# Kernel tuning notes

Hardware: AMD Instinct MI355X
Metric: run time of the kernel (lower is better)

The kernel has to match this reference:

```python
import jax, jax.numpy as jnp
import numpy as np

B, L, D_MODEL = 1, 1024, 768
H = 12            # num_heads == num_key_value_heads
FDIM = 16         # feature_dim
HEAD_DIM = D_MODEL // H  # 64
EPS = 1e-12
R2 = np.sqrt(2.0)
RD = np.sqrt(float(FDIM))        # sqrt(16) = 4
RRD = np.sqrt(RD)                # sqrt(4) = 2


def setup_inputs() -> dict:
    key = jax.random.key(0)
    ks = jax.random.split(key, 5)
    s = 1.0 / np.sqrt(D_MODEL)
    return {
        "hidden_states": jax.random.normal(ks[0], (B, L, D_MODEL), dtype=jnp.float32),
        "Wq": jax.random.normal(ks[1], (D_MODEL, H * FDIM), dtype=jnp.float32) * s,
        "Wk": jax.random.normal(ks[2], (D_MODEL, H * FDIM), dtype=jnp.float32) * s,
        "Wv": jax.random.normal(ks[3], (D_MODEL, D_MODEL), dtype=jnp.float32) * s,
        "Wo": jax.random.normal(ks[4], (D_MODEL, D_MODEL), dtype=jnp.float32) * s,
    }


def taylor_exp_feature_map(x):
    # x: (b, h, l, FDIM) -> (b, h, l, 1 + FDIM + FDIM^2)
    x2 = (x[..., :, None] * x[..., None, :]).reshape(*x.shape[:-1], FDIM * FDIM) / R2
    ones = jnp.ones((*x.shape[:-1], 1), dtype=x.dtype)
    return jnp.concatenate([ones, x / RRD, x2 / RD], axis=-1)


def reference(hidden_states, Wq, Wk, Wv, Wo):
    b, l, _ = hidden_states.shape
    q = (hidden_states @ Wq).reshape(b, l, H, FDIM).transpose(0, 2, 1, 3)
    k = (hidden_states @ Wk).reshape(b, l, H, FDIM).transpose(0, 2, 1, 3)
    v = (hidden_states @ Wv).reshape(b, l, H, HEAD_DIM).transpose(0, 2, 1, 3)
    q = taylor_exp_feature_map(q)  # (b,h,l,Dexp)
    k = taylor_exp_feature_map(k)  # (b,h,l,Dexp)
    # causal linear attention: y_t = q_t . cumsum_t(k_s v_s^T) / (q_t . cumsum_t(k_s) + eps)
    kv = k[..., :, None] * v[..., None, :]          # (b,h,l,Dexp,hd)
    kv_cum = jnp.cumsum(kv, axis=2)                  # (b,h,l,Dexp,hd)
    num = jnp.einsum('bhln,bhlnd->bhld', q, kv_cum)  # (b,h,l,hd)
    k_cum = jnp.cumsum(k, axis=2)                    # (b,h,l,Dexp)
    den = jnp.einsum('bhln,bhln->bhl', q, k_cum)[..., None] + EPS
    y = num / den                                    # (b,h,l,hd)
    y = y.transpose(0, 2, 1, 3).reshape(b, l, H * HEAD_DIM)
    return y @ Wo
```

## Files before the change

kernel.cpp:

```cpp
#include <hip/hip_runtime.h>

#define C2 0.17677669529663687f

typedef __attribute__((ext_vector_type(8))) short short8;
typedef __attribute__((ext_vector_type(8))) unsigned short ushort8;
typedef __attribute__((ext_vector_type(4))) float f32x4;

__device__ __forceinline__ unsigned short f2bf(float x) {
    union { float f; unsigned u; } v; v.f = x;
    unsigned r = v.u + 0x7fffu + ((v.u >> 16) & 1u);
    return (unsigned short)(r >> 16);
}
__device__ __forceinline__ float bf2f(unsigned short u) {
    union { unsigned u; float f; } v; v.u = ((unsigned)u) << 16;
    return v.f;
}

__device__ __forceinline__ void gemm_inblk_splitk(
    const float* __restrict__ A, const float* __restrict__ W,
    float* __restrict__ out, int row0, int n0, int outcol0, int ldw, int outld)
{
    __shared__ unsigned short Al[2][2][64][40];
    __shared__ unsigned short Bl[2][2][64][40];
    __shared__ float red[64][65];
    const int tid = threadIdx.x;
    const int g = tid >> 8;
    const int t = tid & 255;
    const int lane = t & 63, wave4 = t >> 6;
    const int wm = wave4 & 1, wn = wave4 >> 1;
    const int quad = lane >> 4, lr = lane & 15;
    const int k0base = g * 384;

    f32x4 acc[2][2] = {{{0.f,0.f,0.f,0.f},{0.f,0.f,0.f,0.f}},
                       {{0.f,0.f,0.f,0.f},{0.f,0.f,0.f,0.f}}};

    float4 ra[2], rb[2];
    #pragma unroll
    for (int l = 0; l < 2; ++l) {
        int idx = t + l * 256;
        ra[l] = *(const float4*)&A[(size_t)(row0 + (idx >> 3)) * 768 + k0base + (idx & 7) * 4];
        rb[l] = *(const float4*)&W[(size_t)(k0base + (idx >> 4)) * ldw + n0 + (idx & 15) * 4];
    }
    #pragma unroll
    for (int l = 0; l < 2; ++l) {
        int idx = t + l * 256;
        *(ushort4*)&Al[g][0][idx >> 3][(idx & 7) * 4] =
            make_ushort4(f2bf(ra[l].x), f2bf(ra[l].y), f2bf(ra[l].z), f2bf(ra[l].w));
        int kr = idx >> 4, nq = (idx & 15) * 4;
        int col = (((kr >> 3) ^ ((idx & 15) >> 2)) << 3) | (kr & 7);
        Bl[g][0][nq + 0][col] = f2bf(rb[l].x);
        Bl[g][0][nq + 1][col] = f2bf(rb[l].y);
        Bl[g][0][nq + 2][col] = f2bf(rb[l].z);
        Bl[g][0][nq + 3][col] = f2bf(rb[l].w);
    }
    __syncthreads();

    const int ITER = 12;
    #pragma unroll
    for (int i = 0; i < ITER; ++i) {
        const int cur = i & 1, nxt = cur ^ 1;
        float4 na[2], nb[2];
        if (i + 1 < ITER) {
            int kn = k0base + (i + 1) * 32;
            #pragma unroll
            for (int l = 0; l < 2; ++l) {
                int idx = t + l * 256;
                na[l] = *(const float4*)&A[(size_t)(row0 + (idx >> 3)) * 768 + kn + (idx & 7) * 4];
                nb[l] = *(const float4*)&W[(size_t)(kn + (idx >> 4)) * ldw + n0 + (idx & 15) * 4];
            }
        }
        short8 af[2], bfr[2];
        #pragma unroll
        for (int mi = 0; mi < 2; ++mi)
            af[mi] = *(const short8*)&Al[g][cur][wm * 32 + mi * 16 + lr][quad << 3];
        #pragma unroll
        for (int ni = 0; ni < 2; ++ni) {
            int csw = quad ^ ((wn * 2 + ni) & 3);
            bfr[ni] = *(const short8*)&Bl[g][cur][wn * 32 + ni * 16 + lr][csw << 3];
        }
        #pragma unroll
        for (int mi = 0; mi < 2; ++mi)
            #pragma unroll
            for (int ni = 0; ni < 2; ++ni)
                acc[mi][ni] = __builtin_amdgcn_mfma_f32_16x16x32_bf16(af[mi], bfr[ni], acc[mi][ni], 0, 0, 0);
        if (i + 1 < ITER) {
            #pragma unroll
            for (int l = 0; l < 2; ++l) {
                int idx = t + l * 256;
                *(ushort4*)&Al[g][nxt][idx >> 3][(idx & 7) * 4] =
                    make_ushort4(f2bf(na[l].x), f2bf(na[l].y), f2bf(na[l].z), f2bf(na[l].w));
                int kr = idx >> 4, nq = (idx & 15) * 4;
                int col = (((kr >> 3) ^ ((idx & 15) >> 2)) << 3) | (kr & 7);
                Bl[g][nxt][nq + 0][col] = f2bf(nb[l].x);
                Bl[g][nxt][nq + 1][col] = f2bf(nb[l].y);
                Bl[g][nxt][nq + 2][col] = f2bf(nb[l].z);
                Bl[g][nxt][nq + 3][col] = f2bf(nb[l].w);
            }
        }
        __syncthreads();
    }
    if (g == 1) {
        #pragma unroll
        for (int mi = 0; mi < 2; ++mi)
            #pragma unroll
            for (int ni = 0; ni < 2; ++ni)
                #pragma unroll
                for (int r = 0; r < 4; ++r)
                    red[wm * 32 + mi * 16 + quad * 4 + r][wn * 32 + ni * 16 + lr] = acc[mi][ni][r];
    }
    __syncthreads();
    if (g == 0) {
        #pragma unroll
        for (int mi = 0; mi < 2; ++mi)
            #pragma unroll
            for (int ni = 0; ni < 2; ++ni)
                #pragma unroll
                for (int r = 0; r < 4; ++r) {
                    int rr = wm * 32 + mi * 16 + quad * 4 + r;
                    int cc = wn * 32 + ni * 16 + lr;
                    out[(size_t)(row0 + rr) * outld + outcol0 + cc] = acc[mi][ni][r] + red[rr][cc];
                }
    }
}

__global__ __launch_bounds__(512) void gemm_qkv_mfma(
    const float* __restrict__ H, const float* __restrict__ Wq,
    const float* __restrict__ Wk, const float* __restrict__ Wv,
    float* __restrict__ out)
{
    const int nt = blockIdx.x, mt = blockIdx.y;
    const float* W; int ldw, n0;
    if (nt < 3)      { W = Wq; ldw = 192; n0 = nt * 64; }
    else if (nt < 6) { W = Wk; ldw = 192; n0 = (nt - 3) * 64; }
    else             { W = Wv; ldw = 768; n0 = (nt - 6) * 64; }
    gemm_inblk_splitk(H, W, out, mt * 64, n0, nt * 64, ldw, 1152);
}

__global__ __launch_bounds__(512) void gemm_wo_mfma(
    const float* __restrict__ Y, const float* __restrict__ Wo, float* __restrict__ out)
{
    const int nt = blockIdx.x, mt = blockIdx.y;
    gemm_inblk_splitk(Y, Wo, out, mt * 64, nt * 64, nt * 64, 768, 768);
}

__global__ __launch_bounds__(256) void chunk_state_k(
    const float* __restrict__ qkv, unsigned short* __restrict__ St, float* __restrict__ z)
{
    const int c = blockIdx.x, h = blockIdx.y;
    __shared__ float Kc[64][17];
    __shared__ unsigned short Pk[320][72];
    __shared__ unsigned short Vt[80][72];
    const int tid = threadIdx.x;
    const int lane = tid & 63, wave = tid >> 6;
    const int quad = lane >> 4, lr = lane & 15;

    {
        int s = tid >> 2, f4 = (tid & 3) * 4;
        float4 kv = *(const float4*)&qkv[(size_t)(c * 64 + s) * 1152 + 192 + h * 16 + f4];
        Kc[s][f4 + 0] = kv.x; Kc[s][f4 + 1] = kv.y; Kc[s][f4 + 2] = kv.z; Kc[s][f4 + 3] = kv.w;
    }
    #pragma unroll
    for (int l = 0; l < 4; ++l) {
        int idx = tid + l * 256;
        int s = idx >> 4, d4 = (idx & 15) * 4;
        float4 vv = *(const float4*)&qkv[(size_t)(c * 64 + s) * 1152 + 384 + h * 64 + d4];
        Vt[d4 + 0][s] = f2bf(vv.x);
        Vt[d4 + 1][s] = f2bf(vv.y);
        Vt[d4 + 2][s] = f2bf(vv.z);
        Vt[d4 + 3][s] = f2bf(vv.w);
    }
    for (int idx = tid; idx < 16 * 72; idx += 256) {
        int rr = 64 + idx / 72, ss = idx % 72;
        Vt[rr][ss] = (rr == 64 && ss < 64) ? (unsigned short)0x3F80 : (unsigned short)0;
    }
    __syncthreads();
    for (int idx = tid; idx < 2880; idx += 256) {
        int n = idx / 9, s8 = (idx % 9) * 8;
        short8 v8;
        #pragma unroll
        for (int tt = 0; tt < 8; ++tt) {
            int s = s8 + tt;
            float ph = 0.f;
            if (s < 64 && n < 273) {
                if (n == 0) ph = 1.f;
                else if (n < 17) ph = Kc[s][n - 1] * 0.5f;
                else { int m = n - 17; ph = Kc[s][m >> 4] * Kc[s][m & 15] * C2; }
            }
            v8[tt] = (short)f2bf(ph);
        }
        *(short8*)&Pk[n][s8] = v8;
    }
    __syncthreads();

    f32x4 acc[5][5];
    #pragma unroll
    for (int a = 0; a < 5; ++a)
        #pragma unroll
        for (int b = 0; b < 5; ++b) acc[a][b] = (f32x4){0.f, 0.f, 0.f, 0.f};
    #pragma unroll
    for (int ks = 0; ks < 2; ++ks) {
        short8 af[5], bfr[5];
        #pragma unroll
        for (int mt = 0; mt < 5; ++mt)
            af[mt] = *(const short8*)&Vt[mt * 16 + lr][ks * 32 + quad * 8];
        #pragma unroll
        for (int nt = 0; nt < 5; ++nt)
            bfr[nt] = *(const short8*)&Pk[(wave * 5 + nt) * 16 + lr][ks * 32 + quad * 8];
        #pragma unroll
        for (int mt = 0; mt < 5; ++mt)
            #pragma unroll
            for (int nt = 0; nt < 5; ++nt)
                acc[mt][nt] = __builtin_amdgcn_mfma_f32_16x16x32_bf16(af[mt], bfr[nt], acc[mt][nt], 0, 0, 0);
    }
    unsigned short* Sbt = St + (size_t)(h * 16 + c) * 18432;
    float* zb = z + (h * 16 + c) * 273;
    #pragma unroll
    for (int nt = 0; nt < 5; ++nt) {
        int n = (wave * 5 + nt) * 16 + lr;
        if (n < 273) {
            #pragma unroll
            for (int mt = 0; mt < 4; ++mt)
                #pragma unroll
                for (int r = 0; r < 4; ++r)
                    Sbt[(mt * 16 + quad * 4 + r) * 288 + n] = f2bf(acc[mt][nt][r]);
            if (quad == 0) zb[n] = acc[4][nt][0];
        }
    }
}

__global__ __launch_bounds__(256) void scan_state_k(unsigned short* __restrict__ St, float* __restrict__ z)
{
    const int NS = 12 * 64 * 273;
    int e = blockIdx.x * 256 + threadIdx.x;
    if (e < NS) {
        int hh = e / (64 * 273), rem = e % (64 * 273);
        int d = rem / 273, n = rem % 273;
        unsigned short* p = St + (size_t)hh * 16 * 18432 + d * 288 + n;
        float run = 0.f;
        #pragma unroll
        for (int c = 0; c < 16; ++c) {
            float v = bf2f(p[c * 18432]);
            p[c * 18432] = f2bf(run);
            run += v;
        }
    } else if (e < NS + 12 * 273) {
        int e2 = e - NS, hh = e2 / 273, n = e2 % 273;
        float* p = z + hh * 16 * 273 + n;
        float run = 0.f;
        #pragma unroll
        for (int c = 0; c < 16; ++c) { float v = p[c * 273]; p[c * 273] = run; run += v; }
    }
}

__global__ __launch_bounds__(256) void chunk_out_k(
    const float* __restrict__ qkv, const unsigned short* __restrict__ St, const float* __restrict__ z,
    float* __restrict__ y)
{
    const int c = blockIdx.x, h = blockIdx.y;
    __shared__ float Qc[64][17];
    __shared__ unsigned short Aq[64][40];
    __shared__ unsigned short Kb[64][40];
    __shared__ unsigned short Pq[64][360];
    __shared__ unsigned short Sv[64][360];
    __shared__ float zl[288];
    __shared__ float dpart[6][64];
    const int tid = threadIdx.x;
    const int lane = tid & 63, wave = tid >> 6;
    const int wm = wave & 1, wn = wave >> 1;
    const int quad = lane >> 4, lr = lane & 15;

    {
        int s = tid >> 2, f4 = (tid & 3) * 4;
        const float* base = &qkv[(size_t)(c * 64 + s) * 1152 + h * 16];
        float4 qv = *(const float4*)&base[f4];
        float4 kv = *(const float4*)&base[192 + f4];
        Qc[s][f4 + 0] = qv.x; Qc[s][f4 + 1] = qv.y; Qc[s][f4 + 2] = qv.z; Qc[s][f4 + 3] = qv.w;
        *(ushort4*)&Aq[s][f4] = make_ushort4(f2bf(qv.x), f2bf(qv.y), f2bf(qv.z), f2bf(qv.w));
        *(ushort4*)&Kb[s][f4] = make_ushort4(f2bf(kv.x), f2bf(kv.y), f2bf(kv.z), f2bf(kv.w));
        *(ushort4*)&Aq[s][16 + (tid & 3) * 4] = make_ushort4(0, 0, 0, 0);
        *(ushort4*)&Kb[s][16 + (tid & 3) * 4] = make_ushort4(0, 0, 0, 0);
    }
    #pragma unroll
    for (int l = 0; l < 4; ++l) {
        int idx = tid + l * 256;
        int s = idx >> 4, d4 = (idx & 15) * 4;
        float4 vv = *(const float4*)&qkv[(size_t)(c * 64 + s) * 1152 + 384 + h * 64 + d4];
        Sv[d4 + 0][288 + s] = f2bf(vv.x);
        Sv[d4 + 1][288 + s] = f2bf(vv.y);
        Sv[d4 + 2][288 + s] = f2bf(vv.z);
        Sv[d4 + 3][288 + s] = f2bf(vv.w);
    }
    const unsigned short* Sgt = St + (size_t)(h * 16 + c) * 18432;
    for (int idx = tid; idx < 64 * 34; idx += 256) {
        int d = idx / 34, n8 = (idx % 34) * 8;
        *(ushort8*)&Sv[d][n8] = *(const ushort8*)&Sgt[d * 288 + n8];
    }
    for (int idx = tid; idx < 64; idx += 256) Sv[idx][272] = Sgt[idx * 288 + 272];
    for (int idx = tid; idx < 64 * 15; idx += 256) {
        int d = idx / 15, n = 273 + idx % 15;
        Sv[d][n] = 0;
    }
    const float* zg = z + (h * 16 + c) * 273;
    for (int idx = tid; idx < 288; idx += 256) zl[idx] = (idx < 273) ? zg[idx] : 0.f;
    __syncthreads();

    f32x4 accS[2][2] = {{{0.f,0.f,0.f,0.f},{0.f,0.f,0.f,0.f}},
                        {{0.f,0.f,0.f,0.f},{0.f,0.f,0.f,0.f}}};
    {
        short8 af[2], bfr[2];
        #pragma unroll
        for (int mi = 0; mi < 2; ++mi)
            af[mi] = *(const short8*)&Aq[wm * 32 + mi * 16 + lr][quad * 8];
        #pragma unroll
        for (int ni = 0; ni < 2; ++ni)
            bfr[ni] = *(const short8*)&Kb[wn * 32 + ni * 16 + lr][quad * 8];
        #pragma unroll
        for (int mi = 0; mi < 2; ++mi)
            #pragma unroll
            for (int ni = 0; ni < 2; ++ni)
                accS[mi][ni] = __builtin_amdgcn_mfma_f32_16x16x32_bf16(af[mi], bfr[ni], accS[mi][ni], 0, 0, 0);
    }

    {
        int i = lane;
        float qr[16];
        #pragma unroll
        for (int f = 0; f < 16; ++f) qr[f] = Qc[i][f];
        float dp = 0.f;
        int n0 = wave * 72;
        for (int n = n0; n < n0 + 72; ++n) {
            float ph;
            if (n == 0) ph = 1.f;
            else if (n < 17) ph = qr[n - 1] * 0.5f;
            else if (n < 273) { int m = n - 17; ph = qr[m >> 4] * qr[m & 15] * C2; }
            else ph = 0.f;
            Pq[i][n] = f2bf(ph);
            dp += ph * zl[n];
        }
        dpart[wave][i] = dp;
    }

    #pragma unroll
    for (int mi = 0; mi < 2; ++mi) {
        float rs[4] = {0.f, 0.f, 0.f, 0.f};
        #pragma unroll
        for (int ni = 0; ni < 2; ++ni)
            #pragma unroll
            for (int r = 0; r < 4; ++r) {
                int i = wm * 32 + mi * 16 + quad * 4 + r;
                int j = wn * 32 + ni * 16 + lr;
                float u = accS[mi][ni][r];
                float sc = (j <= i) ? (1.f + 0.25f * u + u * u * (1.f / 32.f)) : 0.f;
                rs[r] += sc;
                Pq[i][288 + j] = f2bf(sc);
            }
        #pragma unroll
        for (int r = 0; r < 4; ++r) {
            float v = rs[r];
            v += __shfl_xor(v, 1);
            v += __shfl_xor(v, 2);
            v += __shfl_xor(v, 4);
            v += __shfl_xor(v, 8);
            if (lr == 0) dpart[4 + wn][wm * 32 + mi * 16 + quad * 4 + r] = v;
        }
    }
    __syncthreads();

    f32x4 acc[2][2] = {{{0.f,0.f,0.f,0.f},{0.f,0.f,0.f,0.f}},
                       {{0.f,0.f,0.f,0.f},{0.f,0.f,0.f,0.f}}};
    #pragma unroll
    for (int ks = 0; ks < 11; ++ks) {
        short8 af[2], bfr[2];
        #pragma unroll
        for (int mi = 0; mi < 2; ++mi)
            af[mi] = *(const short8*)&Pq[wm * 32 + mi * 16 + lr][ks * 32 + quad * 8];
        #pragma unroll
        for (int ni = 0; ni < 2; ++ni)
            bfr[ni] = *(const short8*)&Sv[wn * 32 + ni * 16 + lr][ks * 32 + quad * 8];
        #pragma unroll
        for (int mi = 0; mi < 2; ++mi)
            #pragma unroll
            for (int ni = 0; ni < 2; ++ni)
                acc[mi][ni] = __builtin_amdgcn_mfma_f32_16x16x32_bf16(af[mi], bfr[ni], acc[mi][ni], 0, 0, 0);
    }

    #pragma unroll
    for (int mi = 0; mi < 2; ++mi)
        #pragma unroll
        for (int r = 0; r < 4; ++r) {
            int i = wm * 32 + mi * 16 + quad * 4 + r;
            float den = dpart[0][i] + dpart[1][i] + dpart[2][i] +
                        dpart[3][i] + dpart[4][i] + dpart[5][i] + 1e-12f;
            float rden = 1.f / den;
            #pragma unroll
            for (int ni = 0; ni < 2; ++ni)
                y[(size_t)(c * 64 + i) * 768 + h * 64 + wn * 32 + ni * 16 + lr] = acc[mi][ni][r] * rden;
        }
}

extern "C" void kernel_launch(void* const* d_in, const int* in_sizes, int n_in,
                              void* d_out, int out_size, void* d_ws, size_t ws_size,
                              hipStream_t stream) {
    const float* hs = (const float*)d_in[0];
    const float* Wq = (const float*)d_in[1];
    const float* Wk = (const float*)d_in[2];
    const float* Wv = (const float*)d_in[3];
    const float* Wo = (const float*)d_in[4];
    float* out = (float*)d_out;
    float* ws  = (float*)d_ws;

    float* qkv = ws;
    float* yb  = ws + 1179648;
    unsigned short* St = (unsigned short*)(ws + 1966080);
    float* zb  = ws + 5320704;

    gemm_qkv_mfma<<<dim3(18, 16), 512, 0, stream>>>(hs, Wq, Wk, Wv, qkv);
    chunk_state_k<<<dim3(16, 12), 256, 0, stream>>>(qkv, St, zb);
    scan_state_k <<<832, 256, 0, stream>>>(St, zb);
    chunk_out_k  <<<dim3(16, 12), 256, 0, stream>>>(qkv, St, zb, yb);
    gemm_wo_mfma <<<dim3(12, 16), 512, 0, stream>>>(yb, Wo, out);
}
```

Measured before the change: 137.2 us.

## Fuse all five stages into one cooperative persistent kernel with grid syncs

Replaces the five separate launches (QKV GEMM, chunk state, scan, chunk output, Wo GEMM) with one cooperative kernel of 256 blocks that steps through the stages with grid.sync, sharing one union of LDS buffers. The goal is to remove per-launch overhead and the gaps between kernels. To fit the shared-memory union, chunk_out now runs its Pq/Sv feature GEMM in two smaller passes, and chunk_state is spread over 8 waves. The risks are that grid barriers cost time of their own, that the QKV GEMM now needs a second partial round (288 tasks on 256 blocks), and that larger LDS use per block can lower occupancy.

```diff
diff --git a/kernel.cpp b/kernel.cpp
--- a/kernel.cpp
+++ b/kernel.cpp
@@ -1,4 +1,7 @@
 #include <hip/hip_runtime.h>
+#include <hip/hip_cooperative_groups.h>
+
+namespace cg = cooperative_groups;
 
 #define C2 0.17677669529663687f
 
@@ -16,13 +19,16 @@
     return v.f;
 }
 
-__device__ __forceinline__ void gemm_inblk_splitk(
-    const float* __restrict__ A, const float* __restrict__ W,
+struct S1 { unsigned short Al[2][2][64][40]; unsigned short Bl[2][2][64][40]; float red[64][65]; };
+struct S2 { float Kc[64][17]; unsigned short Pk[320][72]; unsigned short Vt[80][72]; };
+struct S4 { float Qc[64][17]; float Kc[64][17]; unsigned short Pq[64][200]; unsigned short Sv[64][200];
+            float zl[288]; float dpart[6][64]; };
+union SMem { S1 s1; S2 s2; S4 s4; };
+
+__device__ __forceinline__ void gemm_body(
+    SMem& sm, const float* __restrict__ A, const float* __restrict__ W,
     float* __restrict__ out, int row0, int n0, int outcol0, int ldw, int outld)
 {
-    __shared__ unsigned short Al[2][2][64][40];
-    __shared__ unsigned short Bl[2][2][64][40];
-    __shared__ float red[64][65];
     const int tid = threadIdx.x;
     const int g = tid >> 8;
     const int t = tid & 255;
@@ -44,14 +50,14 @@
     #pragma unroll
     for (int l = 0; l < 2; ++l) {
         int idx = t + l * 256;
-        *(ushort4*)&Al[g][0][idx >> 3][(idx & 7) * 4] =
+        *(ushort4*)&sm.s1.Al[g][0][idx >> 3][(idx & 7) * 4] =
             make_ushort4(f2bf(ra[l].x), f2bf(ra[l].y), f2bf(ra[l].z), f2bf(ra[l].w));
         int kr = idx >> 4, nq = (idx & 15) * 4;
         int col = (((kr >> 3) ^ ((idx & 15) >> 2)) << 3) | (kr & 7);
-        Bl[g][0][nq + 0][col] = f2bf(rb[l].x);
-        Bl[g][0][nq + 1][col] = f2bf(rb[l].y);
-        Bl[g][0][nq + 2][col] = f2bf(rb[l].z);
-        Bl[g][0][nq + 3][col] = f2bf(rb[l].w);
+        sm.s1.Bl[g][0][nq + 0][col] = f2bf(rb[l].x);
+        sm.s1.Bl[g][0][nq + 1][col] = f2bf(rb[l].y);
+        sm.s1.Bl[g][0][nq + 2][col] = f2bf(rb[l].z);
+        sm.s1.Bl[g][0][nq + 3][col] = f2bf(rb[l].w);
     }
     __syncthreads();
 
@@ -72,11 +78,11 @@
         short8 af[2], bfr[2];
         #pragma unroll
         for (int mi = 0; mi < 2; ++mi)
-            af[mi] = *(const short8*)&Al[g][cur][wm * 32 + mi * 16 + lr][quad << 3];
+            af[mi] = *(const short8*)&sm.s1.Al[g][cur][wm * 32 + mi * 16 + lr][quad << 3];
         #pragma unroll
         for (int ni = 0; ni < 2; ++ni) {
             int csw = quad ^ ((wn * 2 + ni) & 3);
-            bfr[ni] = *(const short8*)&Bl[g][cur][wn * 32 + ni * 16 + lr][csw << 3];
+            bfr[ni] = *(const short8*)&sm.s1.Bl[g][cur][wn * 32 + ni * 16 + lr][csw << 3];
         }
         #pragma unroll
         for (int mi = 0; mi < 2; ++mi)
@@ -87,14 +93,14 @@
             #pragma unroll
             for (int l = 0; l < 2; ++l) {
                 int idx = t + l * 256;
-                *(ushort4*)&Al[g][nxt][idx >> 3][(idx & 7) * 4] =
+                *(ushort4*)&sm.s1.Al[g][nxt][idx >> 3][(idx & 7) * 4] =
                     make_ushort4(f2bf(na[l].x), f2bf(na[l].y), f2bf(na[l].z), f2bf(na[l].w));
                 int kr = idx >> 4, nq = (idx & 15) * 4;
                 int col = (((kr >> 3) ^ ((idx & 15) >> 2)) << 3) | (kr & 7);
-                Bl[g][nxt][nq + 0][col] = f2bf(nb[l].x);
-                Bl[g][nxt][nq + 1][col] = f2bf(nb[l].y);
-                Bl[g][nxt][nq + 2][col] = f2bf(nb[l].z);
-                Bl[g][nxt][nq + 3][col] = f2bf(nb[l].w);
+                sm.s1.Bl[g][nxt][nq + 0][col] = f2bf(nb[l].x);
+                sm.s1.Bl[g][nxt][nq + 1][col] = f2bf(nb[l].y);
+                sm.s1.Bl[g][nxt][nq + 2][col] = f2bf(nb[l].z);
+                sm.s1.Bl[g][nxt][nq + 3][col] = f2bf(nb[l].w);
             }
         }
         __syncthreads();
@@ -106,7 +112,7 @@
             for (int ni = 0; ni < 2; ++ni)
                 #pragma unroll
                 for (int r = 0; r < 4; ++r)
-                    red[wm * 32 + mi * 16 + quad * 4 + r][wn * 32 + ni * 16 + lr] = acc[mi][ni][r];
+                    sm.s1.red[wm * 32 + mi * 16 + quad * 4 + r][wn * 32 + ni * 16 + lr] = acc[mi][ni][r];
     }
     __syncthreads();
     if (g == 0) {
@@ -118,63 +124,43 @@
                 for (int r = 0; r < 4; ++r) {
                     int rr = wm * 32 + mi * 16 + quad * 4 + r;
                     int cc = wn * 32 + ni * 16 + lr;
-                    out[(size_t)(row0 + rr) * outld + outcol0 + cc] = acc[mi][ni][r] + red[rr][cc];
+                    out[(size_t)(row0 + rr) * outld + outcol0 + cc] = acc[mi][ni][r] + sm.s1.red[rr][cc];
                 }
     }
-}
-
-__global__ __launch_bounds__(512) void gemm_qkv_mfma(
-    const float* __restrict__ H, const float* __restrict__ Wq,
-    const float* __restrict__ Wk, const float* __restrict__ Wv,
-    float* __restrict__ out)
+    __syncthreads();
+}
+
+__device__ __forceinline__ void stage_state(
+    SMem& sm, const float* __restrict__ qkv, unsigned short* __restrict__ St,
+    float* __restrict__ z, int task)
 {
-    const int nt = blockIdx.x, mt = blockIdx.y;
-    const float* W; int ldw, n0;
-    if (nt < 3)      { W = Wq; ldw = 192; n0 = nt * 64; }
-    else if (nt < 6) { W = Wk; ldw = 192; n0 = (nt - 3) * 64; }
-    else             { W = Wv; ldw = 768; n0 = (nt - 6) * 64; }
-    gemm_inblk_splitk(H, W, out, mt * 64, n0, nt * 64, ldw, 1152);
-}
-
-__global__ __launch_bounds__(512) void gemm_wo_mfma(
-    const float* __restrict__ Y, const float* __restrict__ Wo, float* __restrict__ out)
-{
-    const int nt = blockIdx.x, mt = blockIdx.y;
-    gemm_inblk_splitk(Y, Wo, out, mt * 64, nt * 64, nt * 64, 768, 768);
-}
-
-__global__ __launch_bounds__(256) void chunk_state_k(
-    const float* __restrict__ qkv, unsigned short* __restrict__ St, float* __restrict__ z)
-{
-    const int c = blockIdx.x, h = blockIdx.y;
-    __shared__ float Kc[64][17];
-    __shared__ unsigned short Pk[320][72];
-    __shared__ unsigned short Vt[80][72];
+    const int h = task >> 4, c = task & 15;
     const int tid = threadIdx.x;
     const int lane = tid & 63, wave = tid >> 6;
     const int quad = lane >> 4, lr = lane & 15;
 
-    {
+    if (tid < 256) {
         int s = tid >> 2, f4 = (tid & 3) * 4;
         float4 kv = *(const float4*)&qkv[(size_t)(c * 64 + s) * 1152 + 192 + h * 16 + f4];
-        Kc[s][f4 + 0] = kv.x; Kc[s][f4 + 1] = kv.y; Kc[s][f4 + 2] = kv.z; Kc[s][f4 + 3] = kv.w;
-    }
-    #pragma unroll
-    for (int l = 0; l < 4; ++l) {
-        int idx = tid + l * 256;
+        sm.s2.Kc[s][f4 + 0] = kv.x; sm.s2.Kc[s][f4 + 1] = kv.y;
+        sm.s2.Kc[s][f4 + 2] = kv.z; sm.s2.Kc[s][f4 + 3] = kv.w;
+    }
+    #pragma unroll
+    for (int l = 0; l < 2; ++l) {
+        int idx = tid + l * 512;
         int s = idx >> 4, d4 = (idx & 15) * 4;
         float4 vv = *(const float4*)&qkv[(size_t)(c * 64 + s) * 1152 + 384 + h * 64 + d4];
-        Vt[d4 + 0][s] = f2bf(vv.x);
-        Vt[d4 + 1][s] = f2bf(vv.y);
-        Vt[d4 + 2][s] = f2bf(vv.z);
-        Vt[d4 + 3][s] = f2bf(vv.w);
-    }
-    for (int idx = tid; idx < 16 * 72; idx += 256) {
+        sm.s2.Vt[d4 + 0][s] = f2bf(vv.x);
+        sm.s2.Vt[d4 + 1][s] = f2bf(vv.y);
+        sm.s2.Vt[d4 + 2][s] = f2bf(vv.z);
+        sm.s2.Vt[d4 + 3][s] = f2bf(vv.w);
+    }
+    for (int idx = tid; idx < 1152; idx += 512) {
         int rr = 64 + idx / 72, ss = idx % 72;
-        Vt[rr][ss] = (rr == 64 && ss < 64) ? (unsigned short)0x3F80 : (unsigned short)0;
-    }
-    __syncthreads();
-    for (int idx = tid; idx < 2880; idx += 256) {
+        sm.s2.Vt[rr][ss] = (rr == 64 && ss < 64) ? (unsigned short)0x3F80 : (unsigned short)0;
+    }
+    __syncthreads();
+    for (int idx = tid; idx < 2880; idx += 512) {
         int n = idx / 9, s8 = (idx % 9) * 8;
         short8 v8;
         #pragma unroll
@@ -183,219 +169,297 @@
             float ph = 0.f;
             if (s < 64 && n < 273) {
                 if (n == 0) ph = 1.f;
-                else if (n < 17) ph = Kc[s][n - 1] * 0.5f;
-                else { int m = n - 17; ph = Kc[s][m >> 4] * Kc[s][m & 15] * C2; }
+                else if (n < 17) ph = sm.s2.Kc[s][n - 1] * 0.5f;
+                else { int m = n - 17; ph = sm.s2.Kc[s][m >> 4] * sm.s2.Kc[s][m & 15] * C2; }
             }
             v8[tt] = (short)f2bf(ph);
         }
-        *(short8*)&Pk[n][s8] = v8;
-    }
-    __syncthreads();
-
-    f32x4 acc[5][5];
-    #pragma unroll
-    for (int a = 0; a < 5; ++a)
+        *(short8*)&sm.s2.Pk[n][s8] = v8;
+    }
+    __syncthreads();
+
+    const int mg = wave & 1, ng = wave >> 1;
+    const int MT = mg ? 2 : 3, mbase = mg ? 3 : 0;
+    f32x4 acc[3][5];
+    #pragma unroll
+    for (int a = 0; a < 3; ++a)
         #pragma unroll
         for (int b = 0; b < 5; ++b) acc[a][b] = (f32x4){0.f, 0.f, 0.f, 0.f};
     #pragma unroll
     for (int ks = 0; ks < 2; ++ks) {
-        short8 af[5], bfr[5];
-        #pragma unroll
-        for (int mt = 0; mt < 5; ++mt)
-            af[mt] = *(const short8*)&Vt[mt * 16 + lr][ks * 32 + quad * 8];
+        short8 af[3], bfr[5];
+        for (int mt = 0; mt < MT; ++mt)
+            af[mt] = *(const short8*)&sm.s2.Vt[(mbase + mt) * 16 + lr][ks * 32 + quad * 8];
         #pragma unroll
         for (int nt = 0; nt < 5; ++nt)
-            bfr[nt] = *(const short8*)&Pk[(wave * 5 + nt) * 16 + lr][ks * 32 + quad * 8];
-        #pragma unroll
-        for (int mt = 0; mt < 5; ++mt)
+            bfr[nt] = *(const short8*)&sm.s2.Pk[(ng * 5 + nt) * 16 + lr][ks * 32 + quad * 8];
+        for (int mt = 0; mt < MT; ++mt)
             #pragma unroll
             for (int nt = 0; nt < 5; ++nt)
                 acc[mt][nt] = __builtin_amdgcn_mfma_f32_16x16x32_bf16(af[mt], bfr[nt], acc[mt][nt], 0, 0, 0);
     }
-    unsigned short* Sbt = St + (size_t)(h * 16 + c) * 18432;
-    float* zb = z + (h * 16 + c) * 273;
+    unsigned short* Sbt = St + (size_t)task * 18432;
+    float* zb = z + (size_t)task * 273;
     #pragma unroll
     for (int nt = 0; nt < 5; ++nt) {
-        int n = (wave * 5 + nt) * 16 + lr;
+        int n = (ng * 5 + nt) * 16 + lr;
         if (n < 273) {
-            #pragma unroll
-            for (int mt = 0; mt < 4; ++mt)
-                #pragma unroll
-                for (int r = 0; r < 4; ++r)
-                    Sbt[(mt * 16 + quad * 4 + r) * 288 + n] = f2bf(acc[mt][nt][r]);
-            if (quad == 0) zb[n] = acc[4][nt][0];
-        }
-    }
-}
-
-__global__ __launch_bounds__(256) void scan_state_k(unsigned short* __restrict__ St, float* __restrict__ z)
+            for (int mt = 0; mt < MT; ++mt) {
+                int mtile = mbase + mt;
+                if (mtile < 4) {
+                    #pragma unroll
+                    for (int r = 0; r < 4; ++r)
+                        Sbt[(mtile * 16 + quad * 4 + r) * 288 + n] = f2bf(acc[mt][nt][r]);
+                } else if (quad == 0) {
+                    zb[n] = acc[mt][nt][0];
+                }
+            }
+        }
+    }
+}
+
+__device__ __forceinline__ void stage_out(
+    SMem& sm, const float* __restrict__ qkv, const unsigned short* __restrict__ St,
+    const float* __restrict__ z, float* __restrict__ y, int task)
 {
-    const int NS = 12 * 64 * 273;
-    int e = blockIdx.x * 256 + threadIdx.x;
-    if (e < NS) {
-        int hh = e / (64 * 273), rem = e % (64 * 273);
-        int d = rem / 273, n = rem % 273;
-        unsigned short* p = St + (size_t)hh * 16 * 18432 + d * 288 + n;
-        float run = 0.f;
-        #pragma unroll
-        for (int c = 0; c < 16; ++c) {
-            float v = bf2f(p[c * 18432]);
-            p[c * 18432] = f2bf(run);
-            run += v;
-        }
-    } else if (e < NS + 12 * 273) {
-        int e2 = e - NS, hh = e2 / 273, n = e2 % 273;
-        float* p = z + hh * 16 * 273 + n;
-        float run = 0.f;
-        #pragma unroll
-        for (int c = 0; c < 16; ++c) { float v = p[c * 273]; p[c * 273] = run; run += v; }
-    }
-}
-
-__global__ __launch_bounds__(256) void chunk_out_k(
-    const float* __restrict__ qkv, const unsigned short* __restrict__ St, const float* __restrict__ z,
-    float* __restrict__ y)
-{
-    const int c = blockIdx.x, h = blockIdx.y;
-    __shared__ float Qc[64][17];
-    __shared__ unsigned short Aq[64][40];
-    __shared__ unsigned short Kb[64][40];
-    __shared__ unsigned short Pq[64][360];
-    __shared__ unsigned short Sv[64][360];
-    __shared__ float zl[288];
-    __shared__ float dpart[6][64];
+    const int h = task >> 4, c = task & 15;
     const int tid = threadIdx.x;
     const int lane = tid & 63, wave = tid >> 6;
-    const int wm = wave & 1, wn = wave >> 1;
+    const int wm = wave & 1, wn = (wave >> 1) & 1;
     const int quad = lane >> 4, lr = lane & 15;
 
-    {
+    if (tid < 256) {
         int s = tid >> 2, f4 = (tid & 3) * 4;
         const float* base = &qkv[(size_t)(c * 64 + s) * 1152 + h * 16];
         float4 qv = *(const float4*)&base[f4];
         float4 kv = *(const float4*)&base[192 + f4];
-        Qc[s][f4 + 0] = qv.x; Qc[s][f4 + 1] = qv.y; Qc[s][f4 + 2] = qv.z; Qc[s][f4 + 3] = qv.w;
-        *(ushort4*)&Aq[s][f4] = make_ushort4(f2bf(qv.x), f2bf(qv.y), f2bf(qv.z), f2bf(qv.w));
-        *(ushort4*)&Kb[s][f4] = make_ushort4(f2bf(kv.x), f2bf(kv.y), f2bf(kv.z), f2bf(kv.w));
-        *(ushort4*)&Aq[s][16 + (tid & 3) * 4] = make_ushort4(0, 0, 0, 0);
-        *(ushort4*)&Kb[s][16 + (tid & 3) * 4] = make_ushort4(0, 0, 0, 0);
-    }
-    #pragma unroll
-    for (int l = 0; l < 4; ++l) {
-        int idx = tid + l * 256;
+        sm.s4.Qc[s][f4 + 0] = qv.x; sm.s4.Qc[s][f4 + 1] = qv.y;
+        sm.s4.Qc[s][f4 + 2] = qv.z; sm.s4.Qc[s][f4 + 3] = qv.w;
+        sm.s4.Kc[s][f4 + 0] = kv.x; sm.s4.Kc[s][f4 + 1] = kv.y;
+        sm.s4.Kc[s][f4 + 2] = kv.z; sm.s4.Kc[s][f4 + 3] = kv.w;
+    }
+    const float* zg = z + (size_t)task * 273;
+    for (int idx = tid; idx < 288; idx += 512) sm.s4.zl[idx] = (idx < 273) ? zg[idx] : 0.f;
+    __syncthreads();
+
+    f32x4 accS[2][2] = {{{0.f,0.f,0.f,0.f},{0.f,0.f,0.f,0.f}},
+                        {{0.f,0.f,0.f,0.f},{0.f,0.f,0.f,0.f}}};
+    float dp = 0.f;
+    if (wave < 4) {
+        short8 afq[2], bfk[2];
+        #pragma unroll
+        for (int mi = 0; mi < 2; ++mi)
+            #pragma unroll
+            for (int j = 0; j < 8; ++j) {
+                int col = quad * 8 + j;
+                afq[mi][j] = (short)((col < 16) ? f2bf(sm.s4.Qc[wm * 32 + mi * 16 + lr][col]) : 0);
+            }
+        #pragma unroll
+        for (int ni = 0; ni < 2; ++ni)
+            #pragma unroll
+            for (int j = 0; j < 8; ++j) {
+                int col = quad * 8 + j;
+                bfk[ni][j] = (short)((col < 16) ? f2bf(sm.s4.Kc[wn * 32 + ni * 16 + lr][col]) : 0);
+            }
+        #pragma unroll
+        for (int mi = 0; mi < 2; ++mi)
+            #pragma unroll
+            for (int ni = 0; ni < 2; ++ni)
+                accS[mi][ni] = __builtin_amdgcn_mfma_f32_16x16x32_bf16(afq[mi], bfk[ni], accS[mi][ni], 0, 0, 0);
+    }
+
+    const unsigned short* Sgt = St + (size_t)task * 18432;
+    #pragma unroll
+    for (int l = 0; l < 3; ++l) {
+        int idx = tid + l * 512;
+        int d = idx / 24, c8 = (idx % 24) * 8;
+        *(ushort8*)&sm.s4.Sv[d][c8] = *(const ushort8*)&Sgt[d * 288 + c8];
+    }
+    if (wave < 4) {
+        float qr[16];
+        #pragma unroll
+        for (int f = 0; f < 16; ++f) qr[f] = sm.s4.Qc[lane][f];
+        for (int l = wave * 48; l < wave * 48 + 48; ++l) {
+            float ph;
+            if (l == 0) ph = 1.f;
+            else if (l < 17) ph = qr[l - 1] * 0.5f;
+            else { int m = l - 17; ph = qr[m >> 4] * qr[m & 15] * C2; }
+            sm.s4.Pq[lane][l] = f2bf(ph);
+            dp += ph * sm.s4.zl[l];
+        }
+    }
+    __syncthreads();
+    f32x4 acc[2][2] = {{{0.f,0.f,0.f,0.f},{0.f,0.f,0.f,0.f}},
+                       {{0.f,0.f,0.f,0.f},{0.f,0.f,0.f,0.f}}};
+    if (wave < 4) {
+        #pragma unroll
+        for (int ks = 0; ks < 6; ++ks) {
+            short8 af[2], bfr[2];
+            #pragma unroll
+            for (int mi = 0; mi < 2; ++mi)
+                af[mi] = *(const short8*)&sm.s4.Pq[wm * 32 + mi * 16 + lr][ks * 32 + quad * 8];
+            #pragma unroll
+            for (int ni = 0; ni < 2; ++ni)
+                bfr[ni] = *(const short8*)&sm.s4.Sv[wn * 32 + ni * 16 + lr][ks * 32 + quad * 8];
+            #pragma unroll
+            for (int mi = 0; mi < 2; ++mi)
+                #pragma unroll
+                for (int ni = 0; ni < 2; ++ni)
+                    acc[mi][ni] = __builtin_amdgcn_mfma_f32_16x16x32_bf16(af[mi], bfr[ni], acc[mi][ni], 0, 0, 0);
+        }
+    }
+    __syncthreads();
+
+    for (int idx = tid; idx < 640; idx += 512) {
+        int d = idx / 10, c8 = (idx % 10) * 8;
+        *(ushort8*)&sm.s4.Sv[d][c8] = *(const ushort8*)&Sgt[d * 288 + 192 + c8];
+    }
+    if (tid < 64) sm.s4.Sv[tid][80] = Sgt[tid * 288 + 272];
+    for (int idx = tid; idx < 960; idx += 512) {
+        int d = idx / 15, n = 81 + idx % 15;
+        sm.s4.Sv[d][n] = 0;
+    }
+    #pragma unroll
+    for (int l = 0; l < 2; ++l) {
+        int idx = tid + l * 512;
         int s = idx >> 4, d4 = (idx & 15) * 4;
         float4 vv = *(const float4*)&qkv[(size_t)(c * 64 + s) * 1152 + 384 + h * 64 + d4];
-        Sv[d4 + 0][288 + s] = f2bf(vv.x);
-        Sv[d4 + 1][288 + s] = f2bf(vv.y);
-        Sv[d4 + 2][288 + s] = f2bf(vv.z);
-        Sv[d4 + 3][288 + s] = f2bf(vv.w);
-    }
-    const unsigned short* Sgt = St + (size_t)(h * 16 + c) * 18432;
-    for (int idx = tid; idx < 64 * 34; idx += 256) {
-        int d = idx / 34, n8 = (idx % 34) * 8;
-        *(ushort8*)&Sv[d][n8] = *(const ushort8*)&Sgt[d * 288 + n8];
-    }
-    for (int idx = tid; idx < 64; idx += 256) Sv[idx][272] = Sgt[idx * 288 + 272];
-    for (int idx = tid; idx < 64 * 15; idx += 256) {
-        int d = idx / 15, n = 273 + idx % 15;
-        Sv[d][n] = 0;
-    }
-    const float* zg = z + (h * 16 + c) * 273;
-    for (int idx = tid; idx < 288; idx += 256) zl[idx] = (idx < 273) ? zg[idx] : 0.f;
-    __syncthreads();
-
-    f32x4 accS[2][2] = {{{0.f,0.f,0.f,0.f},{0.f,0.f,0.f,0.f}},
-                        {{0.f,0.f,0.f,0.f},{0.f,0.f,0.f,0.f}}};
-    {
-        short8 af[2], bfr[2];
-        #pragma unroll
-        for (int mi = 0; mi < 2; ++mi)
-            af[mi] = *(const short8*)&Aq[wm * 32 + mi * 16 + lr][quad * 8];
-        #pragma unroll
-        for (int ni = 0; ni < 2; ++ni)
-            bfr[ni] = *(const short8*)&Kb[wn * 32 + ni * 16 + lr][quad * 8];
-        #pragma unroll
-        for (int mi = 0; mi < 2; ++mi)
-            #pragma unroll
-            for (int ni = 0; ni < 2; ++ni)
-                accS[mi][ni] = __builtin_amdgcn_mfma_f32_16x16x32_bf16(af[mi], bfr[ni], accS[mi][ni], 0, 0, 0);
-    }
-
-    {
-        int i = lane;
+        sm.s4.Sv[d4 + 0][96 + s] = f2bf(vv.x);
+        sm.s4.Sv[d4 + 1][96 + s] = f2bf(vv.y);
+        sm.s4.Sv[d4 + 2][96 + s] = f2bf(vv.z);
+        sm.s4.Sv[d4 + 3][96 + s] = f2bf(vv.w);
+    }
+    if (wave < 4) {
         float qr[16];
         #pragma unroll
-        for (int f = 0; f < 16; ++f) qr[f] = Qc[i][f];
-        float dp = 0.f;
-        int n0 = wave * 72;
-        for (int n = n0; n < n0 + 72; ++n) {
-            float ph;
-            if (n == 0) ph = 1.f;
-            else if (n < 17) ph = qr[n - 1] * 0.5f;
-            else if (n < 273) { int m = n - 17; ph = qr[m >> 4] * qr[m & 15] * C2; }
-            else ph = 0.f;
-            Pq[i][n] = f2bf(ph);
-            dp += ph * zl[n];
-        }
-        dpart[wave][i] = dp;
-    }
-
-    #pragma unroll
-    for (int mi = 0; mi < 2; ++mi) {
-        float rs[4] = {0.f, 0.f, 0.f, 0.f};
-        #pragma unroll
-        for (int ni = 0; ni < 2; ++ni)
+        for (int f = 0; f < 16; ++f) qr[f] = sm.s4.Qc[lane][f];
+        for (int l = wave * 24; l < wave * 24 + 24; ++l) {
+            float ph = 0.f;
+            if (l < 81) {
+                int n = 192 + l, m = n - 17;
+                ph = qr[m >> 4] * qr[m & 15] * C2;
+                dp += ph * sm.s4.zl[n];
+            }
+            sm.s4.Pq[lane][l] = f2bf(ph);
+        }
+        sm.s4.dpart[wave][lane] = dp;
+        #pragma unroll
+        for (int mi = 0; mi < 2; ++mi) {
+            float rs[4] = {0.f, 0.f, 0.f, 0.f};
+            #pragma unroll
+            for (int ni = 0; ni < 2; ++ni)
+                #pragma unroll
+                for (int r = 0; r < 4; ++r) {
+                    int i = wm * 32 + mi * 16 + quad * 4 + r;
+                    int j = wn * 32 + ni * 16 + lr;
+                    float u = accS[mi][ni][r];
+                    float sc = (j <= i) ? (1.f + 0.25f * u + u * u * (1.f / 32.f)) : 0.f;
+                    rs[r] += sc;
+                    sm.s4.Pq[i][96 + j] = f2bf(sc);
+                }
+            #pragma unroll
+            for (int r = 0; r < 4; ++r) {
+                float v = rs[r];
+                v += __shfl_xor(v, 1);
+                v += __shfl_xor(v, 2);
+                v += __shfl_xor(v, 4);
+                v += __shfl_xor(v, 8);
+                if (lr == 0) sm.s4.dpart[4 + wn][wm * 32 + mi * 16 + quad * 4 + r] = v;
+            }
+        }
+    }
+    __syncthreads();
+    if (wave < 4) {
+        #pragma unroll
+        for (int ks = 0; ks < 5; ++ks) {
+            short8 af[2], bfr[2];
+            #pragma unroll
+            for (int mi = 0; mi < 2; ++mi)
+                af[mi] = *(const short8*)&sm.s4.Pq[wm * 32 + mi * 16 + lr][ks * 32 + quad * 8];
+            #pragma unroll
+            for (int ni = 0; ni < 2; ++ni)
+                bfr[ni] = *(const short8*)&sm.s4.Sv[wn * 32 + ni * 16 + lr][ks * 32 + quad * 8];
+            #pragma unroll
+            for (int mi = 0; mi < 2; ++mi)
+                #pragma unroll
+                for (int ni = 0; ni < 2; ++ni)
+                    acc[mi][ni] = __builtin_amdgcn_mfma_f32_16x16x32_bf16(af[mi], bfr[ni], acc[mi][ni], 0, 0, 0);
+        }
+        #pragma unroll
+        for (int mi = 0; mi < 2; ++mi)
             #pragma unroll
             for (int r = 0; r < 4; ++r) {
                 int i = wm * 32 + mi * 16 + quad * 4 + r;
-                int j = wn * 32 + ni * 16 + lr;
-                float u = accS[mi][ni][r];
-                float sc = (j <= i) ? (1.f + 0.25f * u + u * u * (1.f / 32.f)) : 0.f;
-                rs[r] += sc;
-                Pq[i][288 + j] = f2bf(sc);
-            }
-        #pragma unroll
-        for (int r = 0; r < 4; ++r) {
-            float v = rs[r];
-            v += __shfl_xor(v, 1);
-            v += __shfl_xor(v, 2);
-            v += __shfl_xor(v, 4);
-            v += __shfl_xor(v, 8);
-            if (lr == 0) dpart[4 + wn][wm * 32 + mi * 16 + quad * 4 + r] = v;
-        }
-    }
-    __syncthreads();
-
-    f32x4 acc[2][2] = {{{0.f,0.f,0.f,0.f},{0.f,0.f,0.f,0.f}},
-                       {{0.f,0.f,0.f,0.f},{0.f,0.f,0.f,0.f}}};
-    #pragma unroll
-    for (int ks = 0; ks < 11; ++ks) {
-        short8 af[2], bfr[2];
-        #pragma unroll
-        for (int mi = 0; mi < 2; ++mi)
-            af[mi] = *(const short8*)&Pq[wm * 32 + mi * 16 + lr][ks * 32 + quad * 8];
-        #pragma unroll
-        for (int ni = 0; ni < 2; ++ni)
-            bfr[ni] = *(const short8*)&Sv[wn * 32 + ni * 16 + lr][ks * 32 + quad * 8];
-        #pragma unroll
-        for (int mi = 0; mi < 2; ++mi)
-            #pragma unroll
-            for (int ni = 0; ni < 2; ++ni)
-                acc[mi][ni] = __builtin_amdgcn_mfma_f32_16x16x32_bf16(af[mi], bfr[ni], acc[mi][ni], 0, 0, 0);
-    }
-
-    #pragma unroll
-    for (int mi = 0; mi < 2; ++mi)
-        #pragma unroll
-        for (int r = 0; r < 4; ++r) {
-            int i = wm * 32 + mi * 16 + quad * 4 + r;
-            float den = dpart[0][i] + dpart[1][i] + dpart[2][i] +
-                        dpart[3][i] + dpart[4][i] + dpart[5][i] + 1e-12f;
-            float rden = 1.f / den;
-            #pragma unroll
-            for (int ni = 0; ni < 2; ++ni)
-                y[(size_t)(c * 64 + i) * 768 + h * 64 + wn * 32 + ni * 16 + lr] = acc[mi][ni][r] * rden;
-        }
+                float den = sm.s4.dpart[0][i] + sm.s4.dpart[1][i] + sm.s4.dpart[2][i] +
+                            sm.s4.dpart[3][i] + sm.s4.dpart[4][i] + sm.s4.dpart[5][i] + 1e-12f;
+                float rden = 1.f / den;
+                #pragma unroll
+                for (int ni = 0; ni < 2; ++ni)
+                    y[(size_t)(c * 64 + i) * 768 + h * 64 + wn * 32 + ni * 16 + lr] = acc[mi][ni][r] * rden;
+            }
+    }
+    __syncthreads();
+}
+
+__global__ __launch_bounds__(512) void mega_k(
+    const float* __restrict__ hs, const float* __restrict__ Wq, const float* __restrict__ Wk,
+    const float* __restrict__ Wv, const float* __restrict__ Wo,
+    float* __restrict__ out, float* __restrict__ ws)
+{
+    __shared__ SMem sm;
+    cg::grid_group grid = cg::this_grid();
+    float* qkv = ws;
+    float* yb  = ws + 1179648;
+    unsigned short* St = (unsigned short*)(ws + 1966080);
+    float* zb  = ws + 5320704;
+    const int bid = blockIdx.x;
+
+    for (int task = bid; task < 288; task += 256) {
+        int nt = task % 18, mt = task / 18;
+        const float* W; int ldw, n0;
+        if (nt < 3)      { W = Wq; ldw = 192; n0 = nt * 64; }
+        else if (nt < 6) { W = Wk; ldw = 192; n0 = (nt - 3) * 64; }
+        else             { W = Wv; ldw = 768; n0 = (nt - 6) * 64; }
+        gemm_body(sm, hs, W, qkv, mt * 64, n0, nt * 64, ldw, 1152);
+    }
+    grid.sync();
+
+    if (bid < 192) stage_state(sm, qkv, St, zb, bid);
+    grid.sync();
+
+    {
+        const int NS = 12 * 64 * 273;
+        const int total = NS + 12 * 273;
+        for (int e = bid * 512 + threadIdx.x; e < total; e += 131072) {
+            if (e < NS) {
+                int hh = e / (64 * 273), rem = e % (64 * 273);
+                int d = rem / 273, n = rem % 273;
+                unsigned short* p = St + (size_t)hh * 16 * 18432 + d * 288 + n;
+                float run = 0.f;
+                #pragma unroll
+                for (int cc = 0; cc < 16; ++cc) {
+                    float v = bf2f(p[cc * 18432]);
+                    p[cc * 18432] = f2bf(run);
+                    run += v;
+                }
+            } else {
+                int e2 = e - NS, hh = e2 / 273, n = e2 % 273;
+                float* p = zb + (size_t)hh * 16 * 273 + n;
+                float run = 0.f;
+                #pragma unroll
+                for (int cc = 0; cc < 16; ++cc) { float v = p[cc * 273]; p[cc * 273] = run; run += v; }
+            }
+        }
+    }
+    grid.sync();
+
+    if (bid < 192) stage_out(sm, qkv, St, zb, yb, bid);
+    grid.sync();
+
+    if (bid < 192) {
+        int nt = bid % 12, mt = bid / 12;
+        gemm_body(sm, yb, Wo, out, mt * 64, nt * 64, nt * 64, 768, 768);
+    }
 }
 
 extern "C" void kernel_launch(void* const* d_in, const int* in_sizes, int n_in,
@@ -409,14 +473,7 @@
     float* out = (float*)d_out;
     float* ws  = (float*)d_ws;
 
-    float* qkv = ws;
-    float* yb  = ws + 1179648;
-    unsigned short* St = (unsigned short*)(ws + 1966080);
-    float* zb  = ws + 5320704;
-
-    gemm_qkv_mfma<<<dim3(18, 16), 512, 0, stream>>>(hs, Wq, Wk, Wv, qkv);
-    chunk_state_k<<<dim3(16, 12), 256, 0, stream>>>(qkv, St, zb);
-    scan_state_k <<<832, 256, 0, stream>>>(St, zb);
-    chunk_out_k  <<<dim3(16, 12), 256, 0, stream>>>(qkv, St, zb, yb);
-    gemm_wo_mfma <<<dim3(12, 16), 512, 0, stream>>>(yb, Wo, out);
-}
+    void* args[] = { (void*)&hs, (void*)&Wq, (void*)&Wk, (void*)&Wv, (void*)&Wo,
+                     (void*)&out, (void*)&ws };
+    hipLaunchCooperativeKernel((const void*)mega_k, dim3(256), dim3(512), args, 0, stream);
+}
```

Measured after the change: 312.6 us. 128% more time.
